# Kernel optimization log

Measured on AMD Instinct MI355X. Metric: run time of the kernel, lower is better.

The kernel has to match this reference:

```python
import jax, jax.numpy as jnp
import numpy as np

N, P, E, HID = 20000, 12, 640000, 100

def setup_inputs() -> dict:
    key = jax.random.key(0)
    ks = jax.random.split(key, 20)
    inp = {}
    inp['x'] = jax.random.normal(ks[0], (N, P), dtype=jnp.float32)
    inp['edge_index'] = jax.random.randint(ks[1], (2, E), 0, N, dtype=jnp.int64)
    inp['edge_weight'] = jax.random.uniform(ks[2], (E,), dtype=jnp.float32)
    s = 0.1
    # GCNConv weights (in=1, out=HID) and biases for z, r, h gates
    inp['W_z'] = jax.random.normal(ks[3], (1, HID)) * s
    inp['b_z'] = jnp.zeros((HID,))
    inp['W_r'] = jax.random.normal(ks[4], (1, HID)) * s
    inp['b_r'] = jnp.zeros((HID,))
    inp['W_h'] = jax.random.normal(ks[5], (1, HID)) * s
    inp['b_h'] = jnp.zeros((HID,))
    # TGCN linear layers: Linear(2*HID, HID), stored as (in, out)
    inp['Wl_z'] = jax.random.normal(ks[6], (2 * HID, HID)) * s
    inp['bl_z'] = jnp.zeros((HID,))
    inp['Wl_r'] = jax.random.normal(ks[7], (2 * HID, HID)) * s
    inp['bl_r'] = jnp.zeros((HID,))
    inp['Wl_h'] = jax.random.normal(ks[8], (2 * HID, HID)) * s
    inp['bl_h'] = jnp.zeros((HID,))
    # A3TGCN temporal attention logits over periods
    inp['att'] = jax.random.uniform(ks[9], (P,))
    # final Linear(100, 1)
    inp['W_out'] = jax.random.normal(ks[10], (HID, 1)) * s
    inp['b_out'] = jnp.zeros((1,))
    return inp

def _gcn_aggregate(x_np, edge_index, edge_weight):
    # symmetric GCN normalization with self-loops (PyG gcn_norm), then
    # aggregate neighbor features: out[i] = sum_j norm_ij * x[j]
    n = x_np.shape[0]
    src, dst = edge_index[0], edge_index[1]
    loop = jnp.arange(n)
    s = jnp.concatenate([src, loop])
    d = jnp.concatenate([dst, loop])
    w = jnp.concatenate([edge_weight, jnp.ones((n,), dtype=x_np.dtype)])
    deg = jax.ops.segment_sum(w, d, num_segments=n)
    dinv = jnp.where(deg > 0, deg ** -0.5, 0.0)
    norm = dinv[s] * w * dinv[d]                      # (E+N,)
    msgs = norm[:, None] * x_np[s]                    # (E+N, P)
    return jax.ops.segment_sum(msgs, d, num_segments=n)  # (N, P)

def reference(x, edge_index, edge_weight, W_z, b_z, W_r, b_r, W_h, b_h,
              Wl_z, bl_z, Wl_r, bl_r, Wl_h, bl_h, att, W_out, b_out):
    # x: (N, P) -> viewed as (N, in_channels=1, P) in the torch module.
    # GCNConv is linear in x, so aggregate once and apply each gate's weight.
    agg = _gcn_aggregate(x, edge_index, edge_weight)       # (N, P)
    C_z = agg[:, :, None] * W_z[0] + b_z                   # (N, P, HID)
    C_r = agg[:, :, None] * W_r[0] + b_r
    C_h = agg[:, :, None] * W_h[0] + b_h
    # A3TGCN calls TGCN with H=None (zeros) for every period independently.
    H0 = jnp.zeros_like(C_z)
    Z = jax.nn.sigmoid(jnp.concatenate([C_z, H0], -1) @ Wl_z + bl_z)
    R = jax.nn.sigmoid(jnp.concatenate([C_r, H0], -1) @ Wl_r + bl_r)
    Ht = jnp.tanh(jnp.concatenate([C_h, H0 * R], -1) @ Wl_h + bl_h)
    Hp = Z * H0 + (1.0 - Z) * Ht                           # (N, P, HID)
    probs = jax.nn.softmax(att)                            # (P,)
    H_acc = jnp.einsum('npo,p->no', Hp, probs)             # (N, HID)
    h = jax.nn.relu(H_acc)
    return h @ W_out + b_out                               # (N, 1)
```

## Files before the change

kernel.cpp:

```cpp
#include <hip/hip_runtime.h>
#include <hip/hip_bf16.h>

constexpr int N_NODES = 20000;
constexpr int P_PER   = 12;
constexpr int N_EDGES = 640000;
constexpr int HID     = 100;

constexpr int BIN_W   = 64;
constexpr int NB      = (N_NODES + BIN_W - 1) / BIN_W;
constexpr int BCAP    = 2560;
constexpr int NBLK2   = 320;
constexpr int CHUNK   = N_EDGES / NBLK2;
constexpr int CUR_STR = 16;
constexpr int Y_STR   = 16;

constexpr size_t OFF_DINV  = 0;
constexpr size_t OFF_UZ    = OFF_DINV + N_NODES;
constexpr size_t OFF_CZ    = OFF_UZ + HID;
constexpr size_t OFF_UH    = OFF_CZ + HID;
constexpr size_t OFF_CH    = OFF_UH + HID;
constexpr size_t OFF_PROBS = OFF_CH + HID;
constexpr size_t OFF_CUR   = 20416;
constexpr size_t OFF_Y     = OFF_CUR + (size_t)NB * CUR_STR;
constexpr size_t OFF_SEG   = OFF_Y + (size_t)N_NODES * Y_STR;
constexpr size_t OFF_SEG2  = OFF_SEG + (size_t)NB * BCAP * 2;
constexpr size_t OFF_ROW   = OFF_SEG2 + (size_t)NB * BCAP * 2;

__global__ void precompute_kernel(const float* __restrict__ Wz, const float* __restrict__ bz,
                                  const float* __restrict__ Wh, const float* __restrict__ bh,
                                  const float* __restrict__ Wlz, const float* __restrict__ blz,
                                  const float* __restrict__ Wlh, const float* __restrict__ blh,
                                  const float* __restrict__ att,
                                  float* __restrict__ uz, float* __restrict__ cz,
                                  float* __restrict__ uh, float* __restrict__ ch,
                                  float* __restrict__ probs) {
    int t = threadIdx.x;
    if (t < HID) {
        float suz = 0.f, scz = 0.f, suh = 0.f, sch = 0.f;
        for (int j = 0; j < HID; ++j) {
            float wlz = Wlz[j * HID + t];
            float wlh = Wlh[j * HID + t];
            suz += Wz[j] * wlz;
            scz += bz[j] * wlz;
            suh += Wh[j] * wlh;
            sch += bh[j] * wlh;
        }
        uz[t] = suz;
        cz[t] = scz + blz[t];
        uh[t] = suh;
        ch[t] = sch + blh[t];
    }
    if (t == 0) {
        float m = att[0];
        for (int p = 1; p < P_PER; ++p) m = fmaxf(m, att[p]);
        float e[P_PER];
        float s = 0.f;
        for (int p = 0; p < P_PER; ++p) { e[p] = __expf(att[p] - m); s += e[p]; }
        float inv = 1.0f / s;
        for (int p = 0; p < P_PER; ++p) probs[p] = e[p] * inv;
    }
}

__global__ __launch_bounds__(256) void partition_kernel(const int* __restrict__ ei,
                                                        const float* __restrict__ w,
                                                        int* __restrict__ cur,
                                                        int2* __restrict__ seg) {
    __shared__ int hist[NB];
    __shared__ int base[NB];
    __shared__ int run[NB];
    int t = threadIdx.x;
    for (int b = t; b < NB; b += 256) { hist[b] = 0; run[b] = 0; }
    __syncthreads();
    int e0 = blockIdx.x * CHUNK;
    const int* __restrict__ dsts = ei + N_EDGES;
    for (int i = t; i < CHUNK; i += 256) {
        int d = dsts[e0 + i];
        atomicAdd(&hist[d >> 6], 1);
    }
    __syncthreads();
    for (int b = t; b < NB; b += 256) {
        int h = hist[b];
        base[b] = (h > 0) ? atomicAdd(cur + (size_t)b * CUR_STR, h) : 0;
    }
    __syncthreads();
    for (int i = t; i < CHUNK; i += 256) {
        int s = ei[e0 + i];
        int d = dsts[e0 + i];
        float wt = w[e0 + i];
        int b = d >> 6;
        int pos = base[b] + atomicAdd(&run[b], 1);
        if (pos < BCAP)
            seg[(size_t)b * BCAP + pos] = make_int2(s | ((d & 63) << 16), __float_as_int(wt));
    }
}

__global__ __launch_bounds__(256) void binsort_kernel(const int2* __restrict__ seg,
                                                      const int* __restrict__ cur,
                                                      const float* __restrict__ x,
                                                      float* __restrict__ dinv,
                                                      float* __restrict__ y,
                                                      int2* __restrict__ seg2,
                                                      int2* __restrict__ rowinfo) {
    __shared__ int2 ent[BCAP];
    __shared__ int2 ent2[BCAP];
    __shared__ int  hist[BIN_W];
    __shared__ int  off[BIN_W];
    __shared__ int  excl[BIN_W];
    __shared__ float sdinv[BIN_W];
    int t = threadIdx.x;
    int b = blockIdx.x;
    if (t < BIN_W) hist[t] = 0;
    __syncthreads();
    int c = min(cur[(size_t)b * CUR_STR], BCAP);
    const int2* sg = seg + (size_t)b * BCAP;
    for (int i = t; i < c; i += 256) {
        int2 e = sg[i];
        ent[i] = e;
        atomicAdd(&hist[e.x >> 16], 1);
    }
    __syncthreads();
    if (t < 64) {
        int v = hist[t];
        int inc = v;
#pragma unroll
        for (int o = 1; o < 64; o <<= 1) {
            int u = __shfl_up(inc, o, 64);
            if (t >= o) inc += u;
        }
        int ex = inc - v;
        excl[t] = ex;
        off[t]  = ex;
    }
    __syncthreads();
    for (int i = t; i < c; i += 256) {
        int2 e = ent[i];
        int dl = e.x >> 16;
        int p = atomicAdd(&off[dl], 1);
        ent2[p] = make_int2(e.x & 0xFFFF, e.y);
    }
    __syncthreads();
    {
        int nl = t >> 2, l = t & 3;
        int beg = excl[nl];
        int end = beg + hist[nl];
        float s = 0.f;
        for (int j = beg + l; j < end; j += 4) s += __int_as_float(ent2[j].y);
        s += __shfl_xor(s, 1, 64);
        s += __shfl_xor(s, 2, 64);
        if (l == 0) sdinv[nl] = rsqrtf(1.0f + s);
    }
    __syncthreads();
    int n0 = b * BIN_W;
    int2* s2 = seg2 + (size_t)b * BCAP;
    for (int i = t; i < c; i += 256) s2[i] = ent2[i];
    if (t < BIN_W && n0 + t < N_NODES) {
        dinv[n0 + t] = sdinv[t];
        rowinfo[n0 + t] = make_int2(b * BCAP + excl[t], hist[t]);
    }
    for (int i = t; i < BIN_W * P_PER; i += 256) {
        int nl = i / P_PER, p = i - nl * P_PER;
        int n = n0 + nl;
        if (n < N_NODES) y[(size_t)n * Y_STR + p] = sdinv[nl] * x[(size_t)n * P_PER + p];
    }
}

__global__ __launch_bounds__(256) void gather_finalize_kernel(const int2* __restrict__ seg2,
                                                              const int2* __restrict__ rowinfo,
                                                              const float* __restrict__ y,
                                                              const float* __restrict__ dinv,
                                                              const float* __restrict__ uz,
                                                              const float* __restrict__ cz,
                                                              const float* __restrict__ uh,
                                                              const float* __restrict__ ch,
                                                              const float* __restrict__ probs,
                                                              const float* __restrict__ Wout,
                                                              const float* __restrict__ bout,
                                                              float* __restrict__ out) {
    __shared__ float s_uz[HID], s_cz[HID], s_uh[HID], s_ch[HID], s_wo[HID];
    __shared__ float s_pr[P_PER];
    int t = threadIdx.x;
    if (t < HID) {
        s_uz[t] = uz[t]; s_cz[t] = cz[t];
        s_uh[t] = uh[t]; s_ch[t] = ch[t];
        s_wo[t] = Wout[t];
    }
    if (t < P_PER) s_pr[t] = probs[t];
    __syncthreads();

    int tid = blockIdx.x * blockDim.x + t;
    int n = tid >> 4;
    int l = tid & 15;
    if (n >= N_NODES) return;

    int2 ri = rowinfo[n];
    float acc[P_PER];
#pragma unroll
    for (int p = 0; p < P_PER; ++p) acc[p] = 0.f;
    int end = ri.x + ri.y;
    for (int j = ri.x + l; j < end; j += 16) {
        int2 e = seg2[j];
        float wt = __int_as_float(e.y);
        const float4* yr = (const float4*)(y + (size_t)e.x * Y_STR);
        float4 y0 = yr[0], y1 = yr[1], y2 = yr[2];
        acc[0]  += wt * y0.x;  acc[1]  += wt * y0.y;
        acc[2]  += wt * y0.z;  acc[3]  += wt * y0.w;
        acc[4]  += wt * y1.x;  acc[5]  += wt * y1.y;
        acc[6]  += wt * y1.z;  acc[7]  += wt * y1.w;
        acc[8]  += wt * y2.x;  acc[9]  += wt * y2.y;
        acc[10] += wt * y2.z;  acc[11] += wt * y2.w;
    }
#pragma unroll
    for (int off = 8; off >= 1; off >>= 1) {
#pragma unroll
        for (int p = 0; p < P_PER; ++p) acc[p] += __shfl_xor(acc[p], off, 64);
    }
    {
        float dn = dinv[n];
        const float4* yr = (const float4*)(y + (size_t)n * Y_STR);
        float4 y0 = yr[0], y1 = yr[1], y2 = yr[2];
        acc[0]  = dn * (acc[0]  + y0.x);  acc[1]  = dn * (acc[1]  + y0.y);
        acc[2]  = dn * (acc[2]  + y0.z);  acc[3]  = dn * (acc[3]  + y0.w);
        acc[4]  = dn * (acc[4]  + y1.x);  acc[5]  = dn * (acc[5]  + y1.y);
        acc[6]  = dn * (acc[6]  + y1.z);  acc[7]  = dn * (acc[7]  + y1.w);
        acc[8]  = dn * (acc[8]  + y2.x);  acc[9]  = dn * (acc[9]  + y2.y);
        acc[10] = dn * (acc[10] + y2.z);  acc[11] = dn * (acc[11] + y2.w);
    }
    float rk = 0.f;
    for (int k = l; k < HID; k += 16) {
        float uzk = s_uz[k], czk = s_cz[k], uhk = s_uh[k], chk = s_ch[k];
        float a2 = 0.f;
#pragma unroll
        for (int p = 0; p < P_PER; ++p) {
            float av = acc[p];
            float vz = fminf(fmaxf(av * uzk + czk, -30.f), 30.f);
            float vh = fminf(fmaxf(av * uhk + chk, -15.f), 15.f);
            float ez  = __expf(vz);
            float e2h = __expf(2.0f * vh);
            float term = (e2h - 1.0f) / ((1.0f + ez) * (e2h + 1.0f));
            a2 += s_pr[p] * term;
        }
        rk += fmaxf(a2, 0.0f) * s_wo[k];
    }
#pragma unroll
    for (int off = 8; off >= 1; off >>= 1) rk += __shfl_xor(rk, off, 64);
    if (l == 0) out[n] = rk + bout[0];
}

extern "C" void kernel_launch(void* const* d_in, const int* in_sizes, int n_in,
                              void* d_out, int out_size, void* d_ws, size_t ws_size,
                              hipStream_t stream) {
    const float* x   = (const float*)d_in[0];
    const int*   ei  = (const int*)d_in[1];
    const float* ew  = (const float*)d_in[2];
    const float* Wz  = (const float*)d_in[3];
    const float* bz  = (const float*)d_in[4];
    const float* Wh  = (const float*)d_in[7];
    const float* bh  = (const float*)d_in[8];
    const float* Wlz = (const float*)d_in[9];
    const float* blz = (const float*)d_in[10];
    const float* Wlh = (const float*)d_in[13];
    const float* blh = (const float*)d_in[14];
    const float* att = (const float*)d_in[15];
    const float* Wout = (const float*)d_in[16];
    const float* bout = (const float*)d_in[17];
    float* out = (float*)d_out;

    float* ws      = (float*)d_ws;
    float* dinv    = ws + OFF_DINV;
    float* uz      = ws + OFF_UZ;
    float* cz      = ws + OFF_CZ;
    float* uh      = ws + OFF_UH;
    float* ch      = ws + OFF_CH;
    float* probs   = ws + OFF_PROBS;
    int*   cur     = (int*)(ws + OFF_CUR);
    float* y       = ws + OFF_Y;
    int2*  seg     = (int2*)(ws + OFF_SEG);
    int2*  seg2    = (int2*)(ws + OFF_SEG2);
    int2*  rowinfo = (int2*)(ws + OFF_ROW);

    hipMemsetAsync(cur, 0, (size_t)NB * CUR_STR * sizeof(int), stream);
    hipLaunchKernelGGL(precompute_kernel, dim3(1), dim3(128), 0, stream,
                       Wz, bz, Wh, bh, Wlz, blz, Wlh, blh, att, uz, cz, uh, ch, probs);
    hipLaunchKernelGGL(partition_kernel, dim3(NBLK2), dim3(256), 0, stream,
                       ei, ew, cur, seg);
    hipLaunchKernelGGL(binsort_kernel, dim3(NB), dim3(256), 0, stream,
                       seg, cur, x, dinv, y, seg2, rowinfo);
    hipLaunchKernelGGL(gather_finalize_kernel, dim3((N_NODES * 16 + 255) / 256), dim3(256), 0, stream,
                       seg2, rowinfo, y, dinv, uz, cz, uh, ch, probs, Wout, bout, out);
}
```

Baseline: 157.8 us.

## Fuse all stages into one cooperative kernel with grid syncs

Replaces the memset and four separate launches with a single cooperative kernel of 250 blocks. Grid-wide syncs separate the partition, bin-sort, and gather/finalize phases. The sorted edge list stays in shared memory for the gather phase instead of being written back to global, and the small weight precompute is split across blocks as partial sums. This removes launch gaps and intermediate global traffic, but grid.sync costs time and each phase now runs on only 250 blocks with a large shared-memory footprint.

```diff
diff --git a/kernel.cpp b/kernel.cpp
--- a/kernel.cpp
+++ b/kernel.cpp
@@ -1,290 +1,275 @@
 #include <hip/hip_runtime.h>
-#include <hip/hip_bf16.h>
+#include <hip/hip_cooperative_groups.h>
+
+namespace cg = cooperative_groups;
 
 constexpr int N_NODES = 20000;
 constexpr int P_PER   = 12;
 constexpr int N_EDGES = 640000;
 constexpr int HID     = 100;
 
-constexpr int BIN_W   = 64;
-constexpr int NB      = (N_NODES + BIN_W - 1) / BIN_W;
-constexpr int BCAP    = 2560;
-constexpr int NBLK2   = 320;
-constexpr int CHUNK   = N_EDGES / NBLK2;
+constexpr int BIN_W   = 80;
+constexpr int NB      = N_NODES / BIN_W;
+constexpr int BCAP    = 3136;
+constexpr int CHUNK   = N_EDGES / NB;
 constexpr int CUR_STR = 16;
 constexpr int Y_STR   = 16;
-
-constexpr size_t OFF_DINV  = 0;
-constexpr size_t OFF_UZ    = OFF_DINV + N_NODES;
-constexpr size_t OFF_CZ    = OFF_UZ + HID;
-constexpr size_t OFF_UH    = OFF_CZ + HID;
-constexpr size_t OFF_CH    = OFF_UH + HID;
-constexpr size_t OFF_PROBS = OFF_CH + HID;
-constexpr size_t OFF_CUR   = 20416;
-constexpr size_t OFF_Y     = OFF_CUR + (size_t)NB * CUR_STR;
-constexpr size_t OFF_SEG   = OFF_Y + (size_t)N_NODES * Y_STR;
-constexpr size_t OFF_SEG2  = OFF_SEG + (size_t)NB * BCAP * 2;
-constexpr size_t OFF_ROW   = OFF_SEG2 + (size_t)NB * BCAP * 2;
-
-__global__ void precompute_kernel(const float* __restrict__ Wz, const float* __restrict__ bz,
-                                  const float* __restrict__ Wh, const float* __restrict__ bh,
-                                  const float* __restrict__ Wlz, const float* __restrict__ blz,
-                                  const float* __restrict__ Wlh, const float* __restrict__ blh,
-                                  const float* __restrict__ att,
-                                  float* __restrict__ uz, float* __restrict__ cz,
-                                  float* __restrict__ uh, float* __restrict__ ch,
-                                  float* __restrict__ probs) {
-    int t = threadIdx.x;
+constexpr int NPB     = 25;
+constexpr int JPB     = HID / NPB;
+
+constexpr size_t OFF_PART = 0;
+constexpr size_t OFF_CUR  = 10000;
+constexpr size_t OFF_Y    = 14000;
+constexpr size_t OFF_SEG  = OFF_Y + (size_t)N_NODES * Y_STR;
+
+struct EPair { int x, y; };
+
+__global__ __launch_bounds__(256) void fused_all(
+    const float* __restrict__ x,   const int* __restrict__ ei,  const float* __restrict__ ew,
+    const float* __restrict__ Wz,  const float* __restrict__ bz,
+    const float* __restrict__ Wh,  const float* __restrict__ bh,
+    const float* __restrict__ Wlz, const float* __restrict__ blz,
+    const float* __restrict__ Wlh, const float* __restrict__ blh,
+    const float* __restrict__ att, const float* __restrict__ Wout,
+    const float* __restrict__ bout,
+    float* __restrict__ part, int* __restrict__ cur, float* __restrict__ y,
+    EPair* __restrict__ seg, float* __restrict__ out)
+{
+    __shared__ union U {
+        struct { int hist[NB]; int base[NB]; int run[NB]; } p1;
+        EPair ent[BCAP];
+        struct { float uz[HID], cz[HID], uh[HID], ch[HID], wo[HID], pr[P_PER]; } p3;
+    } u;
+    __shared__ EPair ent2[BCAP];
+    __shared__ int   hist[BIN_W], excl[BIN_W], off[BIN_W];
+    __shared__ float sdinv[BIN_W];
+
+    cg::grid_group grid = cg::this_grid();
+    const int t = threadIdx.x;
+    const int b = blockIdx.x;
+
+    if (t == 0) cur[(size_t)b * CUR_STR] = 0;
+    __threadfence();
+    grid.sync();
+
+    if (b < NPB && t < HID) {
+        float suz = 0.f, scz = 0.f, suh = 0.f, sch = 0.f;
+#pragma unroll
+        for (int jj = 0; jj < JPB; ++jj) {
+            int j = b * JPB + jj;
+            float wlz = Wlz[j * HID + t];
+            float wlh = Wlh[j * HID + t];
+            suz += Wz[j] * wlz;  scz += bz[j] * wlz;
+            suh += Wh[j] * wlh;  sch += bh[j] * wlh;
+        }
+        part[(size_t)(4 * b + 0) * HID + t] = suz;
+        part[(size_t)(4 * b + 1) * HID + t] = scz;
+        part[(size_t)(4 * b + 2) * HID + t] = suh;
+        part[(size_t)(4 * b + 3) * HID + t] = sch;
+    }
+    for (int i = t; i < NB; i += 256) { u.p1.hist[i] = 0; u.p1.run[i] = 0; }
+    __syncthreads();
+    const int e0 = b * CHUNK;
+    const int* __restrict__ dsts = ei + N_EDGES;
+    for (int i = t; i < CHUNK; i += 256) {
+        int d = dsts[e0 + i];
+        atomicAdd(&u.p1.hist[d / BIN_W], 1);
+    }
+    __syncthreads();
+    for (int i = t; i < NB; i += 256) {
+        int h = u.p1.hist[i];
+        u.p1.base[i] = (h > 0) ? atomicAdd(cur + (size_t)i * CUR_STR, h) : 0;
+    }
+    __syncthreads();
+    for (int i = t; i < CHUNK; i += 256) {
+        int s  = ei[e0 + i];
+        int d  = dsts[e0 + i];
+        float wt = ew[e0 + i];
+        int bin = d / BIN_W;
+        int dl  = d - bin * BIN_W;
+        int pos = u.p1.base[bin] + atomicAdd(&u.p1.run[bin], 1);
+        if (pos < BCAP) {
+            EPair e; e.x = s | (dl << 16); e.y = __float_as_int(wt);
+            seg[(size_t)bin * BCAP + pos] = e;
+        }
+    }
+    __threadfence();
+    grid.sync();
+    __threadfence();
+
+    if (t < BIN_W) hist[t] = 0;
+    __syncthreads();
+    const int c = min(cur[(size_t)b * CUR_STR], BCAP);
+    const EPair* __restrict__ sg = seg + (size_t)b * BCAP;
+    for (int i = t; i < c; i += 256) {
+        EPair e = sg[i];
+        u.ent[i] = e;
+        atomicAdd(&hist[e.x >> 16], 1);
+    }
+    __syncthreads();
+    if (t < 64) {
+        int v = hist[t], inc = v;
+#pragma unroll
+        for (int o = 1; o < 64; o <<= 1) {
+            int uu = __shfl_up(inc, o, 64);
+            if (t >= o) inc += uu;
+        }
+        excl[t] = inc - v;
+    }
+    __syncthreads();
+    if (t >= 64 && t < BIN_W) {
+        int v = hist[t], inc = v;
+        int lane = t - 64;
+#pragma unroll
+        for (int o = 1; o < 16; o <<= 1) {
+            int uu = __shfl_up(inc, o, 64);
+            if (lane >= o) inc += uu;
+        }
+        excl[t] = (inc - v) + excl[63] + hist[63];
+    }
+    __syncthreads();
+    if (t < BIN_W) off[t] = excl[t];
+    __syncthreads();
+    for (int i = t; i < c; i += 256) {
+        EPair e = u.ent[i];
+        int dl = e.x >> 16;
+        int p  = atomicAdd(&off[dl], 1);
+        EPair o2; o2.x = e.x & 0xFFFF; o2.y = e.y;
+        ent2[p] = o2;
+    }
+    __syncthreads();
+    if (t < BIN_W) {
+        int beg = excl[t], end = excl[t] + hist[t];
+        float s = 0.f;
+        for (int j = beg; j < end; ++j) s += __int_as_float(ent2[j].y);
+        sdinv[t] = rsqrtf(1.0f + s);
+    }
+    __syncthreads();
+    const int n0 = b * BIN_W;
+    for (int i = t; i < BIN_W * P_PER; i += 256) {
+        int nl = i / P_PER, p = i - nl * P_PER;
+        y[(size_t)(n0 + nl) * Y_STR + p] = sdinv[nl] * x[(size_t)(n0 + nl) * P_PER + p];
+    }
+    __threadfence();
+    grid.sync();
+    __threadfence();
+
     if (t < HID) {
         float suz = 0.f, scz = 0.f, suh = 0.f, sch = 0.f;
-        for (int j = 0; j < HID; ++j) {
-            float wlz = Wlz[j * HID + t];
-            float wlh = Wlh[j * HID + t];
-            suz += Wz[j] * wlz;
-            scz += bz[j] * wlz;
-            suh += Wh[j] * wlh;
-            sch += bh[j] * wlh;
-        }
-        uz[t] = suz;
-        cz[t] = scz + blz[t];
-        uh[t] = suh;
-        ch[t] = sch + blh[t];
+        for (int bb = 0; bb < NPB; ++bb) {
+            suz += part[(size_t)(4 * bb + 0) * HID + t];
+            scz += part[(size_t)(4 * bb + 1) * HID + t];
+            suh += part[(size_t)(4 * bb + 2) * HID + t];
+            sch += part[(size_t)(4 * bb + 3) * HID + t];
+        }
+        u.p3.uz[t] = suz;
+        u.p3.cz[t] = scz + blz[t];
+        u.p3.uh[t] = suh;
+        u.p3.ch[t] = sch + blh[t];
+        u.p3.wo[t] = Wout[t];
     }
     if (t == 0) {
         float m = att[0];
         for (int p = 1; p < P_PER; ++p) m = fmaxf(m, att[p]);
-        float e[P_PER];
-        float s = 0.f;
-        for (int p = 0; p < P_PER; ++p) { e[p] = __expf(att[p] - m); s += e[p]; }
-        float inv = 1.0f / s;
-        for (int p = 0; p < P_PER; ++p) probs[p] = e[p] * inv;
-    }
-}
-
-__global__ __launch_bounds__(256) void partition_kernel(const int* __restrict__ ei,
-                                                        const float* __restrict__ w,
-                                                        int* __restrict__ cur,
-                                                        int2* __restrict__ seg) {
-    __shared__ int hist[NB];
-    __shared__ int base[NB];
-    __shared__ int run[NB];
-    int t = threadIdx.x;
-    for (int b = t; b < NB; b += 256) { hist[b] = 0; run[b] = 0; }
-    __syncthreads();
-    int e0 = blockIdx.x * CHUNK;
-    const int* __restrict__ dsts = ei + N_EDGES;
-    for (int i = t; i < CHUNK; i += 256) {
-        int d = dsts[e0 + i];
-        atomicAdd(&hist[d >> 6], 1);
-    }
-    __syncthreads();
-    for (int b = t; b < NB; b += 256) {
-        int h = hist[b];
-        base[b] = (h > 0) ? atomicAdd(cur + (size_t)b * CUR_STR, h) : 0;
-    }
-    __syncthreads();
-    for (int i = t; i < CHUNK; i += 256) {
-        int s = ei[e0 + i];
-        int d = dsts[e0 + i];
-        float wt = w[e0 + i];
-        int b = d >> 6;
-        int pos = base[b] + atomicAdd(&run[b], 1);
-        if (pos < BCAP)
-            seg[(size_t)b * BCAP + pos] = make_int2(s | ((d & 63) << 16), __float_as_int(wt));
-    }
-}
-
-__global__ __launch_bounds__(256) void binsort_kernel(const int2* __restrict__ seg,
-                                                      const int* __restrict__ cur,
-                                                      const float* __restrict__ x,
-                                                      float* __restrict__ dinv,
-                                                      float* __restrict__ y,
-                                                      int2* __restrict__ seg2,
-                                                      int2* __restrict__ rowinfo) {
-    __shared__ int2 ent[BCAP];
-    __shared__ int2 ent2[BCAP];
-    __shared__ int  hist[BIN_W];
-    __shared__ int  off[BIN_W];
-    __shared__ int  excl[BIN_W];
-    __shared__ float sdinv[BIN_W];
-    int t = threadIdx.x;
-    int b = blockIdx.x;
-    if (t < BIN_W) hist[t] = 0;
-    __syncthreads();
-    int c = min(cur[(size_t)b * CUR_STR], BCAP);
-    const int2* sg = seg + (size_t)b * BCAP;
-    for (int i = t; i < c; i += 256) {
-        int2 e = sg[i];
-        ent[i] = e;
-        atomicAdd(&hist[e.x >> 16], 1);
-    }
-    __syncthreads();
-    if (t < 64) {
-        int v = hist[t];
-        int inc = v;
-#pragma unroll
-        for (int o = 1; o < 64; o <<= 1) {
-            int u = __shfl_up(inc, o, 64);
-            if (t >= o) inc += u;
-        }
-        int ex = inc - v;
-        excl[t] = ex;
-        off[t]  = ex;
-    }
-    __syncthreads();
-    for (int i = t; i < c; i += 256) {
-        int2 e = ent[i];
-        int dl = e.x >> 16;
-        int p = atomicAdd(&off[dl], 1);
-        ent2[p] = make_int2(e.x & 0xFFFF, e.y);
-    }
-    __syncthreads();
-    {
-        int nl = t >> 2, l = t & 3;
-        int beg = excl[nl];
-        int end = beg + hist[nl];
-        float s = 0.f;
-        for (int j = beg + l; j < end; j += 4) s += __int_as_float(ent2[j].y);
-        s += __shfl_xor(s, 1, 64);
-        s += __shfl_xor(s, 2, 64);
-        if (l == 0) sdinv[nl] = rsqrtf(1.0f + s);
-    }
-    __syncthreads();
-    int n0 = b * BIN_W;
-    int2* s2 = seg2 + (size_t)b * BCAP;
-    for (int i = t; i < c; i += 256) s2[i] = ent2[i];
-    if (t < BIN_W && n0 + t < N_NODES) {
-        dinv[n0 + t] = sdinv[t];
-        rowinfo[n0 + t] = make_int2(b * BCAP + excl[t], hist[t]);
-    }
-    for (int i = t; i < BIN_W * P_PER; i += 256) {
-        int nl = i / P_PER, p = i - nl * P_PER;
-        int n = n0 + nl;
-        if (n < N_NODES) y[(size_t)n * Y_STR + p] = sdinv[nl] * x[(size_t)n * P_PER + p];
-    }
-}
-
-__global__ __launch_bounds__(256) void gather_finalize_kernel(const int2* __restrict__ seg2,
-                                                              const int2* __restrict__ rowinfo,
-                                                              const float* __restrict__ y,
-                                                              const float* __restrict__ dinv,
-                                                              const float* __restrict__ uz,
-                                                              const float* __restrict__ cz,
-                                                              const float* __restrict__ uh,
-                                                              const float* __restrict__ ch,
-                                                              const float* __restrict__ probs,
-                                                              const float* __restrict__ Wout,
-                                                              const float* __restrict__ bout,
-                                                              float* __restrict__ out) {
-    __shared__ float s_uz[HID], s_cz[HID], s_uh[HID], s_ch[HID], s_wo[HID];
-    __shared__ float s_pr[P_PER];
-    int t = threadIdx.x;
-    if (t < HID) {
-        s_uz[t] = uz[t]; s_cz[t] = cz[t];
-        s_uh[t] = uh[t]; s_ch[t] = ch[t];
-        s_wo[t] = Wout[t];
-    }
-    if (t < P_PER) s_pr[t] = probs[t];
-    __syncthreads();
-
-    int tid = blockIdx.x * blockDim.x + t;
-    int n = tid >> 4;
-    int l = tid & 15;
-    if (n >= N_NODES) return;
-
-    int2 ri = rowinfo[n];
-    float acc[P_PER];
-#pragma unroll
-    for (int p = 0; p < P_PER; ++p) acc[p] = 0.f;
-    int end = ri.x + ri.y;
-    for (int j = ri.x + l; j < end; j += 16) {
-        int2 e = seg2[j];
-        float wt = __int_as_float(e.y);
-        const float4* yr = (const float4*)(y + (size_t)e.x * Y_STR);
-        float4 y0 = yr[0], y1 = yr[1], y2 = yr[2];
-        acc[0]  += wt * y0.x;  acc[1]  += wt * y0.y;
-        acc[2]  += wt * y0.z;  acc[3]  += wt * y0.w;
-        acc[4]  += wt * y1.x;  acc[5]  += wt * y1.y;
-        acc[6]  += wt * y1.z;  acc[7]  += wt * y1.w;
-        acc[8]  += wt * y2.x;  acc[9]  += wt * y2.y;
-        acc[10] += wt * y2.z;  acc[11] += wt * y2.w;
-    }
-#pragma unroll
-    for (int off = 8; off >= 1; off >>= 1) {
-#pragma unroll
-        for (int p = 0; p < P_PER; ++p) acc[p] += __shfl_xor(acc[p], off, 64);
-    }
-    {
-        float dn = dinv[n];
-        const float4* yr = (const float4*)(y + (size_t)n * Y_STR);
-        float4 y0 = yr[0], y1 = yr[1], y2 = yr[2];
-        acc[0]  = dn * (acc[0]  + y0.x);  acc[1]  = dn * (acc[1]  + y0.y);
-        acc[2]  = dn * (acc[2]  + y0.z);  acc[3]  = dn * (acc[3]  + y0.w);
-        acc[4]  = dn * (acc[4]  + y1.x);  acc[5]  = dn * (acc[5]  + y1.y);
-        acc[6]  = dn * (acc[6]  + y1.z);  acc[7]  = dn * (acc[7]  + y1.w);
-        acc[8]  = dn * (acc[8]  + y2.x);  acc[9]  = dn * (acc[9]  + y2.y);
-        acc[10] = dn * (acc[10] + y2.z);  acc[11] = dn * (acc[11] + y2.w);
-    }
-    float rk = 0.f;
-    for (int k = l; k < HID; k += 16) {
-        float uzk = s_uz[k], czk = s_cz[k], uhk = s_uh[k], chk = s_ch[k];
-        float a2 = 0.f;
-#pragma unroll
-        for (int p = 0; p < P_PER; ++p) {
-            float av = acc[p];
-            float vz = fminf(fmaxf(av * uzk + czk, -30.f), 30.f);
-            float vh = fminf(fmaxf(av * uhk + chk, -15.f), 15.f);
-            float ez  = __expf(vz);
-            float e2h = __expf(2.0f * vh);
-            float term = (e2h - 1.0f) / ((1.0f + ez) * (e2h + 1.0f));
-            a2 += s_pr[p] * term;
-        }
-        rk += fmaxf(a2, 0.0f) * s_wo[k];
-    }
-#pragma unroll
-    for (int off = 8; off >= 1; off >>= 1) rk += __shfl_xor(rk, off, 64);
-    if (l == 0) out[n] = rk + bout[0];
+        float e[P_PER]; float ssum = 0.f;
+        for (int p = 0; p < P_PER; ++p) { e[p] = __expf(att[p] - m); ssum += e[p]; }
+        float inv = 1.0f / ssum;
+        for (int p = 0; p < P_PER; ++p) u.p3.pr[p] = e[p] * inv;
+    }
+    __syncthreads();
+
+    const float bo = bout[0];
+    const int l = t & 15;
+    const int g = t >> 4;
+    for (int pass = 0; pass < BIN_W / 16; ++pass) {
+        int nl = pass * 16 + g;
+        int n  = n0 + nl;
+        int beg = excl[nl], len = hist[nl];
+        float acc[P_PER];
+#pragma unroll
+        for (int p = 0; p < P_PER; ++p) acc[p] = 0.f;
+        for (int j = beg + l; j < beg + len; j += 16) {
+            EPair e = ent2[j];
+            float wt = __int_as_float(e.y);
+            const float4* yr = (const float4*)(y + (size_t)e.x * Y_STR);
+            float4 y0 = yr[0], y1 = yr[1], y2 = yr[2];
+            acc[0]  += wt * y0.x;  acc[1]  += wt * y0.y;
+            acc[2]  += wt * y0.z;  acc[3]  += wt * y0.w;
+            acc[4]  += wt * y1.x;  acc[5]  += wt * y1.y;
+            acc[6]  += wt * y1.z;  acc[7]  += wt * y1.w;
+            acc[8]  += wt * y2.x;  acc[9]  += wt * y2.y;
+            acc[10] += wt * y2.z;  acc[11] += wt * y2.w;
+        }
+#pragma unroll
+        for (int o = 8; o >= 1; o >>= 1) {
+#pragma unroll
+            for (int p = 0; p < P_PER; ++p) acc[p] += __shfl_xor(acc[p], o, 64);
+        }
+        {
+            float dn = sdinv[nl];
+            const float4* yr = (const float4*)(y + (size_t)n * Y_STR);
+            float4 y0 = yr[0], y1 = yr[1], y2 = yr[2];
+            acc[0]  = dn * (acc[0]  + y0.x);  acc[1]  = dn * (acc[1]  + y0.y);
+            acc[2]  = dn * (acc[2]  + y0.z);  acc[3]  = dn * (acc[3]  + y0.w);
+            acc[4]  = dn * (acc[4]  + y1.x);  acc[5]  = dn * (acc[5]  + y1.y);
+            acc[6]  = dn * (acc[6]  + y1.z);  acc[7]  = dn * (acc[7]  + y1.w);
+            acc[8]  = dn * (acc[8]  + y2.x);  acc[9]  = dn * (acc[9]  + y2.y);
+            acc[10] = dn * (acc[10] + y2.z);  acc[11] = dn * (acc[11] + y2.w);
+        }
+        float rk = 0.f;
+        for (int k = l; k < HID; k += 16) {
+            float uzk = u.p3.uz[k], czk = u.p3.cz[k];
+            float uhk = u.p3.uh[k], chk = u.p3.ch[k];
+            float a2 = 0.f;
+#pragma unroll
+            for (int p = 0; p < P_PER; ++p) {
+                float av = acc[p];
+                float vz = fminf(fmaxf(av * uzk + czk, -30.f), 30.f);
+                float vh = fminf(fmaxf(av * uhk + chk, -15.f), 15.f);
+                float ez  = __expf(vz);
+                float e2h = __expf(2.0f * vh);
+                float term = (e2h - 1.0f) / ((1.0f + ez) * (e2h + 1.0f));
+                a2 += u.p3.pr[p] * term;
+            }
+            rk += fmaxf(a2, 0.0f) * u.p3.wo[k];
+        }
+#pragma unroll
+        for (int o = 8; o >= 1; o >>= 1) rk += __shfl_xor(rk, o, 64);
+        if (l == 0) out[n] = rk + bo;
+    }
 }
 
 extern "C" void kernel_launch(void* const* d_in, const int* in_sizes, int n_in,
                               void* d_out, int out_size, void* d_ws, size_t ws_size,
                               hipStream_t stream) {
-    const float* x   = (const float*)d_in[0];
-    const int*   ei  = (const int*)d_in[1];
-    const float* ew  = (const float*)d_in[2];
-    const float* Wz  = (const float*)d_in[3];
-    const float* bz  = (const float*)d_in[4];
-    const float* Wh  = (const float*)d_in[7];
-    const float* bh  = (const float*)d_in[8];
-    const float* Wlz = (const float*)d_in[9];
-    const float* blz = (const float*)d_in[10];
-    const float* Wlh = (const float*)d_in[13];
-    const float* blh = (const float*)d_in[14];
-    const float* att = (const float*)d_in[15];
+    (void)in_sizes; (void)n_in; (void)out_size; (void)ws_size;
+    const float* x    = (const float*)d_in[0];
+    const int*   ei   = (const int*)d_in[1];
+    const float* ew   = (const float*)d_in[2];
+    const float* Wz   = (const float*)d_in[3];
+    const float* bz   = (const float*)d_in[4];
+    const float* Wh   = (const float*)d_in[7];
+    const float* bh   = (const float*)d_in[8];
+    const float* Wlz  = (const float*)d_in[9];
+    const float* blz  = (const float*)d_in[10];
+    const float* Wlh  = (const float*)d_in[13];
+    const float* blh  = (const float*)d_in[14];
+    const float* att  = (const float*)d_in[15];
     const float* Wout = (const float*)d_in[16];
     const float* bout = (const float*)d_in[17];
     float* out = (float*)d_out;
 
-    float* ws      = (float*)d_ws;
-    float* dinv    = ws + OFF_DINV;
-    float* uz      = ws + OFF_UZ;
-    float* cz      = ws + OFF_CZ;
-    float* uh      = ws + OFF_UH;
-    float* ch      = ws + OFF_CH;
-    float* probs   = ws + OFF_PROBS;
-    int*   cur     = (int*)(ws + OFF_CUR);
-    float* y       = ws + OFF_Y;
-    int2*  seg     = (int2*)(ws + OFF_SEG);
-    int2*  seg2    = (int2*)(ws + OFF_SEG2);
-    int2*  rowinfo = (int2*)(ws + OFF_ROW);
-
-    hipMemsetAsync(cur, 0, (size_t)NB * CUR_STR * sizeof(int), stream);
-    hipLaunchKernelGGL(precompute_kernel, dim3(1), dim3(128), 0, stream,
-                       Wz, bz, Wh, bh, Wlz, blz, Wlh, blh, att, uz, cz, uh, ch, probs);
-    hipLaunchKernelGGL(partition_kernel, dim3(NBLK2), dim3(256), 0, stream,
-                       ei, ew, cur, seg);
-    hipLaunchKernelGGL(binsort_kernel, dim3(NB), dim3(256), 0, stream,
-                       seg, cur, x, dinv, y, seg2, rowinfo);
-    hipLaunchKernelGGL(gather_finalize_kernel, dim3((N_NODES * 16 + 255) / 256), dim3(256), 0, stream,
-                       seg2, rowinfo, y, dinv, uz, cz, uh, ch, probs, Wout, bout, out);
+    float* ws   = (float*)d_ws;
+    float* part = ws + OFF_PART;
+    int*   cur  = (int*)(ws + OFF_CUR);
+    float* y    = ws + OFF_Y;
+    EPair* seg  = (EPair*)(ws + OFF_SEG);
+
+    void* args[] = { (void*)&x, (void*)&ei, (void*)&ew, (void*)&Wz, (void*)&bz,
+                     (void*)&Wh, (void*)&bh, (void*)&Wlz, (void*)&blz,
+                     (void*)&Wlh, (void*)&blh, (void*)&att, (void*)&Wout,
+                     (void*)&bout, (void*)&part, (void*)&cur, (void*)&y,
+                     (void*)&seg, (void*)&out };
+    hipLaunchCooperativeKernel((const void*)fused_all, dim3(NB), dim3(256),
+                               args, 0, stream);
 }
```

Result: slower. 345.1 us (+118.7%).
